# Performance work log

Hardware: AMD Instinct MI355X
Metric: run time of the kernel (lower is better)

Reference implementation:

```python
import jax, jax.numpy as jnp
import numpy as np
import math

# Static problem sizes (match input_specs)
B, TQ, SQ, TK, SK = 1, 8, 256, 32, 1024
DM, NH = 1024, 8
HD = DM // NH            # 128; mrope_section sums to HD//2
MROPE = [16, 24, 24]
ROPE_BASE = 10000.0


def _build_indices():
    """Reproduce create_idx_cube + slow/fast index selection (all static)."""
    T_max = max(TQ, TK)
    H_max = int(math.sqrt(max(SQ, SK)))
    cube = np.stack(np.meshgrid(np.arange(T_max), np.arange(H_max), np.arange(H_max), indexing='ij'), axis=-1)  # (T,H,W,3)
    # slow (query) indices
    t_idx = np.linspace(0, T_max - 1, TQ).astype(int)
    slow = cube[t_idx]
    if SQ < SK:
        h_q = int(math.sqrt(SQ))
        hi = np.linspace(0, H_max, 2 * h_q + 1).astype(int)[1:-1][::2]
        slow = slow[:, hi][:, :, hi]
    # fast (key) indices
    h_k = int(math.sqrt(SK))
    hf = np.linspace(0, H_max, 2 * h_k + 1).astype(int)[1:-1][::2]
    fast = cube[:, hf][:, :, hf]
    return slow.reshape(-1, 3).T, fast.reshape(-1, 3).T, max(T_max, H_max)


_slow_np, _fast_np, _SEQ = _build_indices()
SLOW_POS = jnp.asarray(_slow_np)   # (3, TQ*SQ) int
FAST_POS = jnp.asarray(_fast_np)   # (3, TK*SK) int

# Standard rotary tables: cos/sin of shape (seq_len, HD)
_inv = 1.0 / (ROPE_BASE ** (np.arange(0, HD, 2, dtype=np.float32) / HD))
_freqs = np.outer(np.arange(_SEQ, dtype=np.float32), _inv)
_emb = np.concatenate([_freqs, _freqs], axis=-1)
COS = jnp.asarray(np.cos(_emb), dtype=jnp.float32)
SIN = jnp.asarray(np.sin(_emb), dtype=jnp.float32)

# per-channel axis (t/h/w) selector, equivalent to the split/concat with i%3
AXIS_MAP = jnp.asarray(np.concatenate([np.full(m, i % 3) for i, m in enumerate(MROPE * 2)]))  # (HD,)


def rotate_half(x):
    return jnp.concatenate([-x[..., HD // 2:], x[..., :HD // 2]], axis=-1)


def apply_mrope(x, pos):
    # x: (B, NH, N, HD); pos: (3, N)
    cos_g = jnp.take_along_axis(COS[pos], AXIS_MAP[None, None, :], axis=0)[0]  # (N, HD)
    sin_g = jnp.take_along_axis(SIN[pos], AXIS_MAP[None, None, :], axis=0)[0]
    return x * cos_g[None, None] + rotate_half(x) * sin_g[None, None]


def setup_inputs() -> dict:
    key = jax.random.key(0)
    ks = jax.random.split(key, 9)
    s = 0.02
    return {
        'q': jax.random.normal(ks[0], (B, TQ, SQ, DM), jnp.float32),
        'k': jax.random.normal(ks[1], (B, TK, SK, DM), jnp.float32),
        'v': jax.random.normal(ks[2], (B, TK, SK, DM), jnp.float32),
        'Wq': jax.random.normal(ks[3], (DM, DM), jnp.float32) * s,
        'bq': jnp.zeros((DM,), jnp.float32),
        'Wk': jax.random.normal(ks[4], (DM, DM), jnp.float32) * s,
        'bk': jnp.zeros((DM,), jnp.float32),
        'Wv': jax.random.normal(ks[5], (DM, DM), jnp.float32) * s,
        'bv': jnp.zeros((DM,), jnp.float32),
    }


def reference(q, k, v, Wq, bq, Wk, bk, Wv, bv):
    # QKV projections -> (B, NH, N, HD)
    qh = (q.reshape(B, TQ * SQ, DM) @ Wq + bq).reshape(B, TQ * SQ, NH, HD).transpose(0, 2, 1, 3)
    kh = (k.reshape(B, TK * SK, DM) @ Wk + bk).reshape(B, TK * SK, NH, HD).transpose(0, 2, 1, 3)
    vh = (v.reshape(B, TK * SK, DM) @ Wv + bv).reshape(B, TK * SK, NH, HD).transpose(0, 2, 1, 3)
    # multimodal 3D RoPE on q (slow frames) and k (fast frames)
    qh = apply_mrope(qh, SLOW_POS)
    kh = apply_mrope(kh, FAST_POS)
    # group time: each query frame attends to its r = TK//TQ aligned kv frames
    r = TK // TQ
    qg = qh.reshape(NH, TQ, SQ, HD).transpose(1, 0, 2, 3)          # (TQ, NH, SQ, HD)
    kg = kh.reshape(NH, TQ, r * SK, HD).transpose(1, 0, 2, 3)      # (TQ, NH, r*SK, HD)
    vg = vh.reshape(NH, TQ, r * SK, HD).transpose(1, 0, 2, 3)
    scores = jnp.einsum('thqd,thkd->thqk', qg, kg) / math.sqrt(HD)
    attn = jax.nn.softmax(scores, axis=-1)
    out = jnp.einsum('thqk,thkd->thqd', attn, vg)                  # (TQ, NH, SQ, HD)
    return out.transpose(0, 2, 1, 3).reshape(B, TQ, SQ, DM)
```

## Files before the change

kernel.cpp:

```cpp
#include <hip/hip_runtime.h>

typedef __bf16 bf16;
typedef __bf16 bf16x8 __attribute__((ext_vector_type(8)));
typedef float  f32x4  __attribute__((ext_vector_type(4)));

#define MFMA16(a, b, c) __builtin_amdgcn_mfma_f32_16x16x32_bf16((a), (b), (c), 0, 0, 0)

#define GLOAD_LDS16(gptr, lptr)                                              \
    __builtin_amdgcn_global_load_lds(                                        \
        (const __attribute__((address_space(1))) unsigned int*)(gptr),       \
        (__attribute__((address_space(3))) unsigned int*)(lptr), 16, 0, 0)

constexpr int kDM = 1024;
constexpr int kNTOK = 32768;

static __device__ inline f32x4 zero4() { f32x4 z = {0.f, 0.f, 0.f, 0.f}; return z; }

__global__ __launch_bounds__(256) void transpose_all(
    const float* __restrict__ Wq, const float* __restrict__ Wk,
    const float* __restrict__ Wv, bf16* __restrict__ Wqt,
    bf16* __restrict__ Wkt, bf16* __restrict__ Wvt)
{
    __shared__ bf16 T[64][68];
    const float* W = (blockIdx.z == 0) ? Wq : (blockIdx.z == 1) ? Wk : Wv;
    bf16* Wt       = (blockIdx.z == 0) ? Wqt : (blockIdx.z == 1) ? Wkt : Wvt;
    const int tid = threadIdx.x;
    const int n0 = blockIdx.x * 64, k0 = blockIdx.y * 64;
    #pragma unroll
    for (int i = 0; i < 4; i++) {
        const int kk = (tid >> 4) + i * 16, nn4 = (tid & 15) * 4;
        float4 v = *(const float4*)&W[(size_t)(k0 + kk) * kDM + n0 + nn4];
        T[nn4 + 0][kk] = (bf16)v.x; T[nn4 + 1][kk] = (bf16)v.y;
        T[nn4 + 2][kk] = (bf16)v.z; T[nn4 + 3][kk] = (bf16)v.w;
    }
    __syncthreads();
    #pragma unroll
    for (int i = 0; i < 4; i++) {
        const int nn = (tid >> 4) + i * 16, kc = (tid & 15) * 4;
        *(ushort4*)&Wt[(size_t)(n0 + nn) * kDM + k0 + kc] = *(const ushort4*)&T[nn][kc];
    }
}

template <int MODE>
__global__ __launch_bounds__(512, 2) void gemm_fused(
    const float* __restrict__ X, const bf16* __restrict__ Wt,
    const float* __restrict__ bias, bf16* __restrict__ out, int mtiles_per_xcd)
{
    __shared__ char smem[131072];

    const int b    = blockIdx.x;
    const int xcd  = b & 7;
    const int s    = b >> 3;
    const int m0   = (xcd * mtiles_per_xcd + (s >> 2)) * 256;
    const int n0   = (s & 3) * 256;
    const int tid  = threadIdx.x;
    const int wave = tid >> 6;
    const int lane = tid & 63;
    const int quad = lane >> 4, l16 = lane & 15;
    const int wr   = wave >> 2;
    const int wc   = wave & 3;

    const int arow  = tid >> 3;
    const int as8   = tid & 7;
    const int awoff = (as8 ^ (arow & 7)) * 8;
    const float* xbase = X + (size_t)(m0 + arow) * kDM + as8 * 8;
    const int bc0 = wave * 4;

    f32x4 acc[8][4];
    #pragma unroll
    for (int i = 0; i < 8; i++)
        #pragma unroll
        for (int j = 0; j < 4; j++) acc[i][j] = zero4();

    {
        #pragma unroll
        for (int i = 0; i < 4; i++) {
            const int row = (bc0 + i) * 8 + (lane >> 3);
            GLOAD_LDS16(&Wt[(size_t)(n0 + row) * kDM + (((lane & 7) ^ (row & 7)) * 8)],
                        (bf16*)(smem + 65536) + (bc0 + i) * 512);
        }
        #pragma unroll
        for (int p = 0; p < 4; p++) {
            const float* src = xbase + (size_t)p * 64 * kDM;
            float4 u0 = *(const float4*)src;
            float4 u1 = *(const float4*)(src + 4);
            bf16x8 w;
            #pragma unroll
            for (int e = 0; e < 4; e++) { w[e] = (bf16)u0[e]; w[4 + e] = (bf16)u1[e]; }
            *(bf16x8*)&((bf16*)smem)[(p * 64 + arow) * 64 + awoff] = w;
        }
        asm volatile("s_waitcnt lgkmcnt(0)" ::: "memory");
        asm volatile("s_waitcnt vmcnt(0)" ::: "memory");
        __builtin_amdgcn_s_barrier();
    }

    for (int t = 0; t < 16; ++t) {
        const int bt = t & 1;
        bf16* Ac = (bf16*)(smem + bt * 32768);
        bf16* An = (bf16*)(smem + (bt ^ 1) * 32768);
        bf16* Bc = (bf16*)(smem + 65536 + bt * 32768);
        bf16* Bn = (bf16*)(smem + 65536 + (bt ^ 1) * 32768);

        float4 av[8];
        if (t < 15) {
            const int k1 = (t + 1) * 64;
            #pragma unroll
            for (int p = 0; p < 4; p++) {
                const float* src = xbase + (size_t)p * 64 * kDM + k1;
                av[p * 2]     = *(const float4*)src;
                av[p * 2 + 1] = *(const float4*)(src + 4);
            }
            #pragma unroll
            for (int i = 0; i < 4; i++) {
                const int row = (bc0 + i) * 8 + (lane >> 3);
                GLOAD_LDS16(&Wt[(size_t)(n0 + row) * kDM + k1 + (((lane & 7) ^ (row & 7)) * 8)],
                            Bn + (bc0 + i) * 512);
            }
        }
        __builtin_amdgcn_sched_barrier(0);

        #pragma unroll
        for (int ks = 0; ks < 2; ++ks) {
            bf16x8 a[8], bq[4];
            const int G = ks * 4 + quad;
            #pragma unroll
            for (int i = 0; i < 8; i++)
                a[i] = *(const bf16x8*)&Ac[(wr * 128 + i * 16 + l16) * 64 + ((G ^ (l16 & 7)) * 8)];
            #pragma unroll
            for (int j = 0; j < 4; j++)
                bq[j] = *(const bf16x8*)&Bc[(wc * 64 + j * 16 + l16) * 64 + ((G ^ (l16 & 7)) * 8)];
            #pragma unroll
            for (int i = 0; i < 8; i++)
                #pragma unroll
                for (int j = 0; j < 4; j++)
                    acc[i][j] = MFMA16(a[i], bq[j], acc[i][j]);
        }

        if (t < 15) {
            #pragma unroll
            for (int p = 0; p < 4; p++) {
                bf16x8 w;
                #pragma unroll
                for (int e = 0; e < 4; e++) {
                    w[e]     = (bf16)av[p * 2][e];
                    w[4 + e] = (bf16)av[p * 2 + 1][e];
                }
                *(bf16x8*)&An[(p * 64 + arow) * 64 + awoff] = w;
            }
        }
        asm volatile("s_waitcnt lgkmcnt(0)" ::: "memory");
        asm volatile("s_waitcnt vmcnt(0)" ::: "memory");
        __builtin_amdgcn_s_barrier();
    }

    if (MODE == 3) {
        bf16* Y3 = (bf16*)smem;
        #pragma unroll
        for (int h = 0; h < 2; h++) {
            if ((wc >> 1) == h) {
                #pragma unroll
                for (int j = 0; j < 4; j++) {
                    const int nl = (wc & 1) * 64 + j * 16 + l16;
                    const float bv = bias[n0 + wc * 64 + j * 16 + l16];
                    #pragma unroll
                    for (int i = 0; i < 8; i++) {
                        bf16 tmp[4];
                        #pragma unroll
                        for (int r = 0; r < 4; r++) tmp[r] = (bf16)(acc[i][j][r] + bv);
                        *(ushort4*)&Y3[nl * 264 + wr * 128 + i * 16 + quad * 4] =
                            *(const ushort4*)tmp;
                    }
                }
            }
            __syncthreads();
            const int nl = tid >> 5, m8 = (tid & 31) * 8;
            #pragma unroll
            for (int kk = 0; kk < 8; kk++)
                *(uint4*)&out[(size_t)(n0 + h * 128 + nl + kk * 16) * kNTOK + m0 + m8] =
                    *(const uint4*)&Y3[(nl + kk * 16) * 264 + m8];
            __syncthreads();
        }
    } else {
        bf16* Y = (bf16*)smem;
        #pragma unroll
        for (int h = 0; h < 2; h++) {
            if ((wc >> 1) == h && (wc & 1)) {
                #pragma unroll
                for (int j = 0; j < 4; j++) {
                    const int dj = j * 16 + l16;
                    const float bv = bias[n0 + wc * 64 + j * 16 + l16];
                    #pragma unroll
                    for (int i = 0; i < 8; i++)
                        #pragma unroll
                        for (int r = 0; r < 4; r++)
                            Y[(wr * 128 + i * 16 + quad * 4 + r) * 136 + 64 + dj] =
                                (bf16)(acc[i][j][r] + bv);
                }
            }
            __syncthreads();
            if ((wc >> 1) == h && !(wc & 1)) {
                #pragma unroll
                for (int j = 0; j < 4; j++) {
                    const int d = j * 16 + l16;
                    const float bv = bias[n0 + wc * 64 + j * 16 + l16];
                    const float invf = exp2f((float)d * -0.20762050593045951f);
                    #pragma unroll
                    for (int i = 0; i < 8; i++) {
                        #pragma unroll
                        for (int r = 0; r < 4; r++) {
                            const int mloc = wr * 128 + i * 16 + quad * 4 + r;
                            const int tok = m0 + mloc;
                            int pt, ph, pw;
                            if (MODE == 2) { pt = tok >> 10; ph = (tok >> 5) & 31; pw = tok & 31; }
                            else { int tq = tok >> 8; pt = (31 * tq) / 7;
                                   ph = 2 * ((tok >> 4) & 15) + 1; pw = 2 * (tok & 15) + 1; }
                            const int p = (d < 16) ? pt : ((d < 40) ? ph : pw);
                            float sn, cs;
                            __sincosf((float)p * invf, &sn, &cs);
                            const float x1 = acc[i][j][r] + bv;
                            const float x2 = (float)Y[mloc * 136 + 64 + d];
                            Y[mloc * 136 + d]      = (bf16)(x1 * cs - x2 * sn);
                            Y[mloc * 136 + 64 + d] = (bf16)(x2 * cs + x1 * sn);
                        }
                    }
                }
            }
            __syncthreads();
            const int rrow = tid >> 1, seg = (tid & 1) * 64;
            #pragma unroll
            for (int kk = 0; kk < 8; kk++)
                *(uint4*)&out[(size_t)(m0 + rrow) * kDM + n0 + h * 128 + seg + kk * 8] =
                    *(const uint4*)&Y[rrow * 136 + seg + kk * 8];
            __syncthreads();
        }
    }
}

__global__ __launch_bounds__(256) void attn_kernel(
    const bf16* __restrict__ qh, const bf16* __restrict__ kh,
    const bf16* __restrict__ vt, float* __restrict__ Opart, float* __restrict__ ml)
{
    __shared__ bf16 Ks[64 * 128];
    __shared__ bf16 Vs[128 * 64];
    __shared__ bf16 Ps[4][16][64];

    const int tid  = threadIdx.x;
    const int z    = blockIdx.x, h = blockIdx.y, qb = blockIdx.z;
    const int t    = z >> 2, sp = z & 3;
    const int wave = tid >> 6;
    const int lane = tid & 63;
    const int quad = lane >> 4, l16 = lane & 15;

    const int qrow = qb * 64 + wave * 16 + l16;
    const size_t qbase = ((size_t)(t * 256 + qrow)) * kDM + h * 128;
    bf16x8 aq[4];
    #pragma unroll
    for (int kb = 0; kb < 4; kb++)
        aq[kb] = *(const bf16x8*)&qh[qbase + kb * 32 + quad * 8];

    bf16x8 ones;
    #pragma unroll
    for (int e = 0; e < 8; e++) ones[e] = (bf16)1.0f;

    f32x4 o[9];
    #pragma unroll
    for (int j = 0; j < 9; j++) o[j] = zero4();
    float m_run[4];
    #pragma unroll
    for (int r = 0; r < 4; r++) m_run[r] = -1e30f;
    const float scale = 0.08838834764831845f;

    const int r16 = lane >> 4, j16 = lane & 15;
    const int r8  = lane >> 3, j8  = lane & 7;

    for (int kt = 0; kt < 16; kt++) {
        const int kbase = t * 4096 + sp * 1024 + kt * 64;
        __syncthreads();
        #pragma unroll
        for (int i = 0; i < 4; i++) {
            const int c = wave * 4 + i;
            const int krow = c * 4 + r16;
            GLOAD_LDS16(&kh[(size_t)(kbase + krow) * kDM + h * 128 + ((j16 ^ (krow & 15)) * 8)],
                        &Ks[c * 512]);
        }
        #pragma unroll
        for (int i = 0; i < 4; i++) {
            const int c = wave * 4 + i;
            GLOAD_LDS16(&vt[(size_t)(h * 128 + c * 8 + r8) * kNTOK + kbase + ((j8 ^ r8) * 8)],
                        &Vs[c * 512]);
        }
        __syncthreads();

        f32x4 s[4];
        #pragma unroll
        for (int c = 0; c < 4; c++) s[c] = zero4();
        #pragma unroll
        for (int kb = 0; kb < 4; kb++) {
            #pragma unroll
            for (int c = 0; c < 4; c++) {
                bf16x8 b = *(const bf16x8*)&Ks[(c * 16 + l16) * 128 + (((kb * 4 + quad) ^ l16) * 8)];
                s[c] = MFMA16(aq[kb], b, s[c]);
            }
        }

        float alpha[4];
        #pragma unroll
        for (int r = 0; r < 4; r++) {
            float sv[4];
            #pragma unroll
            for (int c = 0; c < 4; c++) sv[c] = s[c][r] * scale;
            float mx = fmaxf(fmaxf(sv[0], sv[1]), fmaxf(sv[2], sv[3]));
            #pragma unroll
            for (int off = 1; off < 16; off <<= 1) mx = fmaxf(mx, __shfl_xor(mx, off));
            const float mn = fmaxf(m_run[r], mx);
            alpha[r] = __expf(m_run[r] - mn);
            m_run[r] = mn;
            const int q7 = quad * 4 + r;
            #pragma unroll
            for (int c = 0; c < 4; c++) {
                const int col = (c * 16 + l16) ^ ((q7 & 7) * 8);
                Ps[wave][q7][col] = (bf16)__expf(sv[c] - mn);
            }
        }
        #pragma unroll
        for (int j = 0; j < 9; j++)
            #pragma unroll
            for (int r = 0; r < 4; r++) o[j][r] *= alpha[r];
        #pragma unroll
        for (int ks = 0; ks < 2; ks++) {
            bf16x8 pa = *(const bf16x8*)&Ps[wave][l16][((ks * 4 + quad) ^ (l16 & 7)) * 8];
            #pragma unroll
            for (int j = 0; j < 8; j++) {
                bf16x8 bv = *(const bf16x8*)&Vs[(j * 16 + l16) * 64 + (((ks * 4 + quad) ^ (l16 & 7)) * 8)];
                o[j] = MFMA16(pa, bv, o[j]);
            }
            o[8] = MFMA16(pa, ones, o[8]);
        }
    }

    #pragma unroll
    for (int r = 0; r < 4; r++) {
        const int srow = qb * 64 + wave * 16 + quad * 4 + r;
        const size_t pr = ((size_t)(z * 8 + h)) * 256 + srow;
        #pragma unroll
        for (int j = 0; j < 8; j++)
            Opart[pr * 128 + j * 16 + l16] = o[j][r];
        if (l16 == 0) { ml[pr * 2] = m_run[r]; ml[pr * 2 + 1] = o[8][r]; }
    }
}

__global__ __launch_bounds__(256) void combine_kernel(
    const float* __restrict__ Opart, const float* __restrict__ ml,
    float* __restrict__ out)
{
    const int tid = threadIdx.x;
    const int rid = blockIdx.x * 2 + (tid >> 7);
    const int d   = tid & 127;
    const int t = rid >> 11, h = (rid >> 8) & 7, srow = rid & 255;

    float mv[4], lv[4];
    #pragma unroll
    for (int sp = 0; sp < 4; sp++) {
        const size_t pr = ((size_t)((t * 4 + sp) * 8 + h)) * 256 + srow;
        float2 p = *(const float2*)&ml[pr * 2];
        mv[sp] = p.x; lv[sp] = p.y;
    }
    const float ms = fmaxf(fmaxf(mv[0], mv[1]), fmaxf(mv[2], mv[3]));
    float lsum = 0.f, acc = 0.f;
    #pragma unroll
    for (int sp = 0; sp < 4; sp++) {
        const size_t pr = ((size_t)((t * 4 + sp) * 8 + h)) * 256 + srow;
        const float w = __expf(mv[sp] - ms);
        lsum += lv[sp] * w;
        acc  += Opart[pr * 128 + d] * w;
    }
    out[((size_t)(t * 256 + srow)) * kDM + h * 128 + d] = acc / lsum;
}

extern "C" void kernel_launch(void* const* d_in, const int* in_sizes, int n_in,
                              void* d_out, int out_size, void* d_ws, size_t ws_size,
                              hipStream_t stream)
{
    const float* q  = (const float*)d_in[0];
    const float* k  = (const float*)d_in[1];
    const float* v  = (const float*)d_in[2];
    const float* Wq = (const float*)d_in[3];
    const float* bq = (const float*)d_in[4];
    const float* Wk = (const float*)d_in[5];
    const float* bk = (const float*)d_in[6];
    const float* Wv = (const float*)d_in[7];
    const float* bv = (const float*)d_in[8];
    float* out = (float*)d_out;

    bf16* qh  = (bf16*)d_ws;
    bf16* kh  = qh + (size_t)2048 * 1024;
    bf16* vt  = kh + (size_t)32768 * 1024;
    bf16* Wqt = vt + (size_t)32768 * 1024;
    bf16* Wkt = Wqt + (size_t)1024 * 1024;
    bf16* Wvt = Wkt + (size_t)1024 * 1024;
    float* Opart = (float*)(Wvt + (size_t)1024 * 1024);
    float* ml    = Opart + (size_t)32 * 8 * 256 * 128;

    transpose_all<<<dim3(16, 16, 3), 256, 0, stream>>>(Wq, Wk, Wv, Wqt, Wkt, Wvt);
    gemm_fused<1><<<32,  512, 0, stream>>>(q, Wqt, bq, qh, 1);
    gemm_fused<2><<<512, 512, 0, stream>>>(k, Wkt, bk, kh, 16);
    gemm_fused<3><<<512, 512, 0, stream>>>(v, Wvt, bv, vt, 16);
    attn_kernel<<<dim3(32, 8, 4), 256, 0, stream>>>(qh, kh, vt, Opart, ml);
    combine_kernel<<<8192, 256, 0, stream>>>(Opart, ml, out);
}
```

Measured before the change: 650.5 us.

## Merge QKV GEMMs into one launch, triple-buffer weight tiles, prioritize attention MFMAs

Replaces the three templated projection GEMM launches with a single 1056-block kernel that picks Q/K/V operands at runtime from the block index. This removes launch gaps and per-launch tail effects. Weight tiles are now triple-buffered in LDS and prefetched two steps ahead, with partial vmcnt waits, so the global-to-LDS loads overlap more of the MFMA work. The A-tile conversion store is placed between the two k-substeps. In the attention kernel, s_setprio raises wave priority around the MFMA blocks. The cost is 160KB of LDS per block and a runtime mode branch in the epilogue.

Result: no change. 659.5 us (+1.4%).

```diff
diff --git a/kernel.cpp b/kernel.cpp
--- a/kernel.cpp
+++ b/kernel.cpp
@@ -41,17 +41,26 @@
     }
 }
 
-template <int MODE>
-__global__ __launch_bounds__(512, 2) void gemm_fused(
-    const float* __restrict__ X, const bf16* __restrict__ Wt,
-    const float* __restrict__ bias, bf16* __restrict__ out, int mtiles_per_xcd)
+__global__ __launch_bounds__(512, 2) void gemm_fused_all(
+    const float* __restrict__ Xq, const float* __restrict__ Xk,
+    const float* __restrict__ Xv, const bf16* __restrict__ Wqt,
+    const bf16* __restrict__ Wkt, const bf16* __restrict__ Wvt,
+    const float* __restrict__ bq, const float* __restrict__ bk,
+    const float* __restrict__ bv, bf16* __restrict__ qh,
+    bf16* __restrict__ kh, bf16* __restrict__ vt)
 {
-    __shared__ char smem[131072];
-
-    const int b    = blockIdx.x;
+    __shared__ char smem[163840];
+
+    int b = blockIdx.x;
+    const float* X; const bf16* Wt; const float* bias; bf16* out;
+    int mtiles, mode;
+    if (b < 512)       { X = Xk; Wt = Wkt; bias = bk; out = kh; mtiles = 16; mode = 2; }
+    else if (b < 1024) { b -= 512; X = Xv; Wt = Wvt; bias = bv; out = vt; mtiles = 16; mode = 3; }
+    else               { b -= 1024; X = Xq; Wt = Wqt; bias = bq; out = qh; mtiles = 1; mode = 1; }
+
     const int xcd  = b & 7;
     const int s    = b >> 3;
-    const int m0   = (xcd * mtiles_per_xcd + (s >> 2)) * 256;
+    const int m0   = (xcd * mtiles + (s >> 2)) * 256;
     const int n0   = (s & 3) * 256;
     const int tid  = threadIdx.x;
     const int wave = tid >> 6;
@@ -72,34 +81,66 @@
         #pragma unroll
         for (int j = 0; j < 4; j++) acc[i][j] = zero4();
 
-    {
+    auto stageB = [&](int kk, char* dst) {
         #pragma unroll
         for (int i = 0; i < 4; i++) {
             const int row = (bc0 + i) * 8 + (lane >> 3);
-            GLOAD_LDS16(&Wt[(size_t)(n0 + row) * kDM + (((lane & 7) ^ (row & 7)) * 8)],
-                        (bf16*)(smem + 65536) + (bc0 + i) * 512);
-        }
+            GLOAD_LDS16(&Wt[(size_t)(n0 + row) * kDM + kk + (((lane & 7) ^ (row & 7)) * 8)],
+                        (bf16*)dst + (bc0 + i) * 512);
+        }
+    };
+    auto computeKs = [&](const bf16* Ac, const bf16* Bc, int ks) {
+        bf16x8 a[8], bfr[4];
+        const int G = ks * 4 + quad;
+        #pragma unroll
+        for (int i = 0; i < 8; i++)
+            a[i] = *(const bf16x8*)&Ac[(wr * 128 + i * 16 + l16) * 64 + ((G ^ (l16 & 7)) * 8)];
+        #pragma unroll
+        for (int j = 0; j < 4; j++)
+            bfr[j] = *(const bf16x8*)&Bc[(wc * 64 + j * 16 + l16) * 64 + ((G ^ (l16 & 7)) * 8)];
+        #pragma unroll
+        for (int i = 0; i < 8; i++)
+            #pragma unroll
+            for (int j = 0; j < 4; j++)
+                acc[i][j] = MFMA16(a[i], bfr[j], acc[i][j]);
+    };
+
+    {
+        stageB(0, smem + 65536);
+        __builtin_amdgcn_sched_barrier(0);
+        float4 av[8];
         #pragma unroll
         for (int p = 0; p < 4; p++) {
             const float* src = xbase + (size_t)p * 64 * kDM;
-            float4 u0 = *(const float4*)src;
-            float4 u1 = *(const float4*)(src + 4);
+            av[p * 2]     = *(const float4*)src;
+            av[p * 2 + 1] = *(const float4*)(src + 4);
+        }
+        __builtin_amdgcn_sched_barrier(0);
+        stageB(64, smem + 98304);
+        __builtin_amdgcn_sched_barrier(0);
+        asm volatile("s_waitcnt vmcnt(4)" ::: "memory");
+        bf16* A0 = (bf16*)smem;
+        #pragma unroll
+        for (int p = 0; p < 4; p++) {
             bf16x8 w;
             #pragma unroll
-            for (int e = 0; e < 4; e++) { w[e] = (bf16)u0[e]; w[4 + e] = (bf16)u1[e]; }
-            *(bf16x8*)&((bf16*)smem)[(p * 64 + arow) * 64 + awoff] = w;
+            for (int e = 0; e < 4; e++) {
+                w[e]     = (bf16)av[p * 2][e];
+                w[4 + e] = (bf16)av[p * 2 + 1][e];
+            }
+            *(bf16x8*)&A0[(p * 64 + arow) * 64 + awoff] = w;
         }
         asm volatile("s_waitcnt lgkmcnt(0)" ::: "memory");
-        asm volatile("s_waitcnt vmcnt(0)" ::: "memory");
+        __builtin_amdgcn_sched_barrier(0);
         __builtin_amdgcn_s_barrier();
     }
 
+    int c3 = 0, p3 = 2;
     for (int t = 0; t < 16; ++t) {
-        const int bt = t & 1;
-        bf16* Ac = (bf16*)(smem + bt * 32768);
-        bf16* An = (bf16*)(smem + (bt ^ 1) * 32768);
-        bf16* Bc = (bf16*)(smem + 65536 + bt * 32768);
-        bf16* Bn = (bf16*)(smem + 65536 + (bt ^ 1) * 32768);
+        const bf16* Ac = (const bf16*)(smem + (t & 1) * 32768);
+        bf16*       An = (bf16*)(smem + ((t + 1) & 1) * 32768);
+        const bf16* Bc = (const bf16*)(smem + 65536 + c3 * 32768);
+        char*       Bp = smem + 65536 + p3 * 32768;
 
         float4 av[8];
         if (t < 15) {
@@ -110,31 +151,12 @@
                 av[p * 2]     = *(const float4*)src;
                 av[p * 2 + 1] = *(const float4*)(src + 4);
             }
-            #pragma unroll
-            for (int i = 0; i < 4; i++) {
-                const int row = (bc0 + i) * 8 + (lane >> 3);
-                GLOAD_LDS16(&Wt[(size_t)(n0 + row) * kDM + k1 + (((lane & 7) ^ (row & 7)) * 8)],
-                            Bn + (bc0 + i) * 512);
-            }
-        }
-        __builtin_amdgcn_sched_barrier(0);
-
-        #pragma unroll
-        for (int ks = 0; ks < 2; ++ks) {
-            bf16x8 a[8], bq[4];
-            const int G = ks * 4 + quad;
-            #pragma unroll
-            for (int i = 0; i < 8; i++)
-                a[i] = *(const bf16x8*)&Ac[(wr * 128 + i * 16 + l16) * 64 + ((G ^ (l16 & 7)) * 8)];
-            #pragma unroll
-            for (int j = 0; j < 4; j++)
-                bq[j] = *(const bf16x8*)&Bc[(wc * 64 + j * 16 + l16) * 64 + ((G ^ (l16 & 7)) * 8)];
-            #pragma unroll
-            for (int i = 0; i < 8; i++)
-                #pragma unroll
-                for (int j = 0; j < 4; j++)
-                    acc[i][j] = MFMA16(a[i], bq[j], acc[i][j]);
-        }
+        }
+        __builtin_amdgcn_sched_barrier(0);
+        if (t < 14) stageB((t + 2) * 64, Bp);
+        __builtin_amdgcn_sched_barrier(0);
+
+        computeKs(Ac, Bc, 0);
 
         if (t < 15) {
             #pragma unroll
@@ -148,12 +170,19 @@
                 *(bf16x8*)&An[(p * 64 + arow) * 64 + awoff] = w;
             }
         }
+
+        computeKs(Ac, Bc, 1);
+
+        if (t < 14) asm volatile("s_waitcnt vmcnt(4)" ::: "memory");
+        else        asm volatile("s_waitcnt vmcnt(0)" ::: "memory");
         asm volatile("s_waitcnt lgkmcnt(0)" ::: "memory");
-        asm volatile("s_waitcnt vmcnt(0)" ::: "memory");
+        __builtin_amdgcn_sched_barrier(0);
         __builtin_amdgcn_s_barrier();
-    }
-
-    if (MODE == 3) {
+        c3 = (c3 == 2) ? 0 : c3 + 1;
+        p3 = (p3 == 2) ? 0 : p3 + 1;
+    }
+
+    if (mode == 3) {
         bf16* Y3 = (bf16*)smem;
         #pragma unroll
         for (int h = 0; h < 2; h++) {
@@ -211,7 +240,7 @@
                             const int mloc = wr * 128 + i * 16 + quad * 4 + r;
                             const int tok = m0 + mloc;
                             int pt, ph, pw;
-                            if (MODE == 2) { pt = tok >> 10; ph = (tok >> 5) & 31; pw = tok & 31; }
+                            if (mode == 2) { pt = tok >> 10; ph = (tok >> 5) & 31; pw = tok & 31; }
                             else { int tq = tok >> 8; pt = (31 * tq) / 7;
                                    ph = 2 * ((tok >> 4) & 15) + 1; pw = 2 * (tok & 15) + 1; }
                             const int p = (d < 16) ? pt : ((d < 40) ? ph : pw);
@@ -294,6 +323,7 @@
         f32x4 s[4];
         #pragma unroll
         for (int c = 0; c < 4; c++) s[c] = zero4();
+        __builtin_amdgcn_s_setprio(1);
         #pragma unroll
         for (int kb = 0; kb < 4; kb++) {
             #pragma unroll
@@ -302,6 +332,7 @@
                 s[c] = MFMA16(aq[kb], b, s[c]);
             }
         }
+        __builtin_amdgcn_s_setprio(0);
 
         float alpha[4];
         #pragma unroll
@@ -326,6 +357,7 @@
         for (int j = 0; j < 9; j++)
             #pragma unroll
             for (int r = 0; r < 4; r++) o[j][r] *= alpha[r];
+        __builtin_amdgcn_s_setprio(1);
         #pragma unroll
         for (int ks = 0; ks < 2; ks++) {
             bf16x8 pa = *(const bf16x8*)&Ps[wave][l16][((ks * 4 + quad) ^ (l16 & 7)) * 8];
@@ -336,6 +368,7 @@
             }
             o[8] = MFMA16(pa, ones, o[8]);
         }
+        __builtin_amdgcn_s_setprio(0);
     }
 
     #pragma unroll
@@ -402,9 +435,8 @@
     float* ml    = Opart + (size_t)32 * 8 * 256 * 128;
 
     transpose_all<<<dim3(16, 16, 3), 256, 0, stream>>>(Wq, Wk, Wv, Wqt, Wkt, Wvt);
-    gemm_fused<1><<<32,  512, 0, stream>>>(q, Wqt, bq, qh, 1);
-    gemm_fused<2><<<512, 512, 0, stream>>>(k, Wkt, bk, kh, 16);
-    gemm_fused<3><<<512, 512, 0, stream>>>(v, Wvt, bv, vt, 16);
+    gemm_fused_all<<<1056, 512, 0, stream>>>(q, k, v, Wqt, Wkt, Wvt,
+                                             bq, bk, bv, qh, kh, vt);
     attn_kernel<<<dim3(32, 8, 4), 256, 0, stream>>>(qh, kh, vt, Opart, ml);
     combine_kernel<<<8192, 256, 0, stream>>>(Opart, ml, out);
 }
```
